# Kernel tuning notes

Measured on AMD Instinct MI355X. Metric: run time of the kernel, lower is better.

The kernel has to match this reference:

```python
import jax, jax.numpy as jnp
import numpy as np

D = 256          # volume side
N_LABELS = 1000  # number of distinct vessel IDs (0 = background)


def setup_inputs() -> dict:
    key = jax.random.key(0)
    k1, k2, k3, k4 = jax.random.split(key, 4)
    vessel_labels = jax.random.randint(k1, (D, D, D), 0, N_LABELS, dtype=jnp.int32)
    keep_mask = jax.random.randint(k2, (N_LABELS,), 0, 2, dtype=jnp.int32)
    # per-label intensity in [0, 0.7) or [1.3, 2) depending on a coin flip,
    # matching sample_label_intensity's Uniform(0,0.7) / Uniform(1.3,2)
    u = jax.random.uniform(k3, (N_LABELS,))
    coin = jax.random.bernoulli(k4, 0.5, (N_LABELS,))
    intensity_lut = jnp.where(coin, 1.3 + 0.7 * u, 0.7 * u).astype(jnp.float32)
    parenchyma = jax.random.uniform(jax.random.fold_in(key, 9), (D, D, D), dtype=jnp.float32)
    return {
        "vessel_labels": vessel_labels,
        "keep_mask": keep_mask,
        "intensity_lut": intensity_lut,
        "parenchyma": parenchyma,
    }


def reference(vessel_labels, keep_mask, intensity_lut, parenchyma):
    # prune_labels: hide labels whose keep_mask is 0 (set them to background 0)
    keep = keep_mask[vessel_labels] > 0          # [D,D,D] bool, single gather
    labels = jnp.where(keep, vessel_labels, 0)   # pruned label volume

    # sample_label_intensity as a LUT gather: O(voxels) instead of
    # O(labels * voxels) masked_fill_ loop. Background (label 0) -> 1.0.
    lut = intensity_lut.at[0].set(jnp.float32(1.0))
    vessel_intensities = lut[labels]             # [D,D,D] float32

    # vessel mask = labels.clip(0, 1).to(int16)
    vessel_mask = (labels > 0).astype(jnp.int16)

    # parenchyma[mask>0] *= intensities[mask>0]
    out = parenchyma * jnp.where(vessel_mask > 0, vessel_intensities, jnp.float32(1.0))
    return out, vessel_mask
```

## Files before the change

### kernel.cpp

```cpp
#include <hip/hip_runtime.h>

#define DVOL 256
#define NVOX (DVOL * DVOL * DVOL)
#define N_LABELS 1000

#define BLOCK   256
#define UNROLL  8
#define NGROUPS (NVOX / 4)
#define NBLOCKS (NGROUPS / (BLOCK * UNROLL))

typedef float f32x4 __attribute__((ext_vector_type(4)));
typedef int   i32x4 __attribute__((ext_vector_type(4)));

__global__ __launch_bounds__(BLOCK)
void vessel_fuse_kernel(const int* __restrict__ labels,
                        const int* __restrict__ keep_mask,
                        const float* __restrict__ intensity_lut,
                        const float* __restrict__ parenchyma,
                        float* __restrict__ out,
                        float* __restrict__ maskf)
{
    __shared__ float s_scale[N_LABELS];

    for (int l = threadIdx.x; l < N_LABELS; l += BLOCK) {
        const bool keep = (l > 0) && (keep_mask[l] > 0);
        s_scale[l] = keep ? intensity_lut[l] : 1.0f;
    }
    __syncthreads();

    const i32x4* lab4 = (const i32x4*)labels;
    const f32x4* par4 = (const f32x4*)parenchyma;
    f32x4* out4 = (f32x4*)out;
    f32x4* msk4 = (f32x4*)maskf;

    const int base = blockIdx.x * (BLOCK * UNROLL) + threadIdx.x;

    i32x4 L[UNROLL];
    f32x4 P[UNROLL];
#pragma unroll
    for (int k = 0; k < UNROLL; ++k) {
        L[k] = lab4[base + k * BLOCK];
        P[k] = par4[base + k * BLOCK];
    }
    __builtin_amdgcn_sched_barrier(0);

#pragma unroll
    for (int k = 0; k < UNROLL; ++k) {
        const int idx = base + k * BLOCK;

        f32x4 s;
        s.x = s_scale[L[k].x];
        s.y = s_scale[L[k].y];
        s.z = s_scale[L[k].z];
        s.w = s_scale[L[k].w];

        f32x4 o, m;
        o.x = P[k].x * s.x;  m.x = (s.x != 1.0f) ? 1.0f : 0.0f;
        o.y = P[k].y * s.y;  m.y = (s.y != 1.0f) ? 1.0f : 0.0f;
        o.z = P[k].z * s.z;  m.z = (s.z != 1.0f) ? 1.0f : 0.0f;
        o.w = P[k].w * s.w;  m.w = (s.w != 1.0f) ? 1.0f : 0.0f;

        __builtin_nontemporal_store(o, &out4[idx]);
        __builtin_nontemporal_store(m, &msk4[idx]);
    }
}

extern "C" void kernel_launch(void* const* d_in, const int* in_sizes, int n_in,
                              void* d_out, int out_size, void* d_ws, size_t ws_size,
                              hipStream_t stream) {
    (void)in_sizes; (void)n_in; (void)d_ws; (void)ws_size; (void)out_size;

    const int*   vessel_labels = (const int*)d_in[0];
    const int*   keep_mask     = (const int*)d_in[1];
    const float* intensity_lut = (const float*)d_in[2];
    const float* parenchyma    = (const float*)d_in[3];

    float* out   = (float*)d_out;
    float* maskf = (float*)d_out + NVOX;

    vessel_fuse_kernel<<<NBLOCKS, BLOCK, 0, stream>>>(
        vessel_labels, keep_mask, intensity_lut, parenchyma, out, maskf);
}
```

Measured before the change: 240.5 us.

## Precompute fused LUT in workspace kernel and gather from global/L2 per voxel

```diff
diff --git a/kernel.cpp b/kernel.cpp
--- a/kernel.cpp
+++ b/kernel.cpp
@@ -5,23 +5,60 @@
 #define N_LABELS 1000
 
 #define BLOCK   256
-#define UNROLL  8
 #define NGROUPS (NVOX / 4)
-#define NBLOCKS (NGROUPS / (BLOCK * UNROLL))
+#define NBLOCKS (NGROUPS / BLOCK)
 
 typedef float f32x4 __attribute__((ext_vector_type(4)));
 typedef int   i32x4 __attribute__((ext_vector_type(4)));
 
 __global__ __launch_bounds__(BLOCK)
+void build_fused_lut(const int* __restrict__ keep_mask,
+                     const float* __restrict__ intensity_lut,
+                     float* __restrict__ fused)
+{
+    for (int l = threadIdx.x; l < N_LABELS; l += BLOCK) {
+        const bool keep = (l > 0) && (keep_mask[l] > 0);
+        fused[l] = keep ? intensity_lut[l] : 1.0f;
+    }
+}
+
+__global__ __launch_bounds__(BLOCK)
 void vessel_fuse_kernel(const int* __restrict__ labels,
-                        const int* __restrict__ keep_mask,
-                        const float* __restrict__ intensity_lut,
+                        const float* __restrict__ fused,
                         const float* __restrict__ parenchyma,
                         float* __restrict__ out,
                         float* __restrict__ maskf)
 {
+    const int i = blockIdx.x * BLOCK + threadIdx.x;
+
+    const i32x4 L = __builtin_nontemporal_load((const i32x4*)labels + i);
+    const f32x4 P = __builtin_nontemporal_load((const f32x4*)parenchyma + i);
+
+    f32x4 s;
+    s.x = fused[L.x];
+    s.y = fused[L.y];
+    s.z = fused[L.z];
+    s.w = fused[L.w];
+
+    f32x4 o, m;
+    o.x = P.x * s.x;  m.x = (s.x != 1.0f) ? 1.0f : 0.0f;
+    o.y = P.y * s.y;  m.y = (s.y != 1.0f) ? 1.0f : 0.0f;
+    o.z = P.z * s.z;  m.z = (s.z != 1.0f) ? 1.0f : 0.0f;
+    o.w = P.w * s.w;  m.w = (s.w != 1.0f) ? 1.0f : 0.0f;
+
+    __builtin_nontemporal_store(o, (f32x4*)out + i);
+    __builtin_nontemporal_store(m, (f32x4*)maskf + i);
+}
+
+__global__ __launch_bounds__(BLOCK)
+void vessel_fuse_lds(const int* __restrict__ labels,
+                     const int* __restrict__ keep_mask,
+                     const float* __restrict__ intensity_lut,
+                     const float* __restrict__ parenchyma,
+                     float* __restrict__ out,
+                     float* __restrict__ maskf)
+{
     __shared__ float s_scale[N_LABELS];
-
     for (int l = threadIdx.x; l < N_LABELS; l += BLOCK) {
         const bool keep = (l > 0) && (keep_mask[l] > 0);
         s_scale[l] = keep ? intensity_lut[l] : 1.0f;
@@ -33,42 +70,26 @@
     f32x4* out4 = (f32x4*)out;
     f32x4* msk4 = (f32x4*)maskf;
 
-    const int base = blockIdx.x * (BLOCK * UNROLL) + threadIdx.x;
-
-    i32x4 L[UNROLL];
-    f32x4 P[UNROLL];
-#pragma unroll
-    for (int k = 0; k < UNROLL; ++k) {
-        L[k] = lab4[base + k * BLOCK];
-        P[k] = par4[base + k * BLOCK];
-    }
-    __builtin_amdgcn_sched_barrier(0);
-
-#pragma unroll
-    for (int k = 0; k < UNROLL; ++k) {
-        const int idx = base + k * BLOCK;
-
-        f32x4 s;
-        s.x = s_scale[L[k].x];
-        s.y = s_scale[L[k].y];
-        s.z = s_scale[L[k].z];
-        s.w = s_scale[L[k].w];
-
-        f32x4 o, m;
-        o.x = P[k].x * s.x;  m.x = (s.x != 1.0f) ? 1.0f : 0.0f;
-        o.y = P[k].y * s.y;  m.y = (s.y != 1.0f) ? 1.0f : 0.0f;
-        o.z = P[k].z * s.z;  m.z = (s.z != 1.0f) ? 1.0f : 0.0f;
-        o.w = P[k].w * s.w;  m.w = (s.w != 1.0f) ? 1.0f : 0.0f;
-
-        __builtin_nontemporal_store(o, &out4[idx]);
-        __builtin_nontemporal_store(m, &msk4[idx]);
+    const int stride = gridDim.x * blockDim.x;
+    for (int i = blockIdx.x * BLOCK + threadIdx.x; i < NGROUPS; i += stride) {
+        const i32x4 L = lab4[i];
+        const f32x4 P = par4[i];
+        f32x4 s, o, m;
+        s.x = s_scale[L.x]; s.y = s_scale[L.y];
+        s.z = s_scale[L.z]; s.w = s_scale[L.w];
+        o.x = P.x * s.x;  m.x = (s.x != 1.0f) ? 1.0f : 0.0f;
+        o.y = P.y * s.y;  m.y = (s.y != 1.0f) ? 1.0f : 0.0f;
+        o.z = P.z * s.z;  m.z = (s.z != 1.0f) ? 1.0f : 0.0f;
+        o.w = P.w * s.w;  m.w = (s.w != 1.0f) ? 1.0f : 0.0f;
+        out4[i] = o;
+        msk4[i] = m;
     }
 }
 
 extern "C" void kernel_launch(void* const* d_in, const int* in_sizes, int n_in,
                               void* d_out, int out_size, void* d_ws, size_t ws_size,
                               hipStream_t stream) {
-    (void)in_sizes; (void)n_in; (void)d_ws; (void)ws_size; (void)out_size;
+    (void)in_sizes; (void)n_in; (void)out_size;
 
     const int*   vessel_labels = (const int*)d_in[0];
     const int*   keep_mask     = (const int*)d_in[1];
@@ -78,6 +99,13 @@
     float* out   = (float*)d_out;
     float* maskf = (float*)d_out + NVOX;
 
-    vessel_fuse_kernel<<<NBLOCKS, BLOCK, 0, stream>>>(
-        vessel_labels, keep_mask, intensity_lut, parenchyma, out, maskf);
+    if (d_ws != nullptr && ws_size >= N_LABELS * sizeof(float)) {
+        float* fused = (float*)d_ws;
+        build_fused_lut<<<1, BLOCK, 0, stream>>>(keep_mask, intensity_lut, fused);
+        vessel_fuse_kernel<<<NBLOCKS, BLOCK, 0, stream>>>(
+            vessel_labels, fused, parenchyma, out, maskf);
+    } else {
+        vessel_fuse_lds<<<4096, BLOCK, 0, stream>>>(
+            vessel_labels, keep_mask, intensity_lut, parenchyma, out, maskf);
+    }
 }
```

Measured after the change: 230.4 us, median of 2. 4.2% less time.
